# Kernel optimization log

Hardware: AMD Instinct MI355X
Metric: run time of the kernel (lower is better)

## Reference

```python
import jax, jax.numpy as jnp
import numpy as np

C = 0.01            # curvature, hard-coded in the original forward
TEMPERATURE = 0.5
SCALE_BY_TEMPERATURE = True
ARTANH_CLAMP = 1.0 - 1e-5


def setup_inputs() -> dict:
    key = jax.random.key(0)
    k1, k2 = jax.random.split(key)
    B, D = 4096, 128
    features = jax.random.uniform(k1, (B, D), dtype=jnp.float32)
    labels = jax.random.randint(k2, (B,), 0, 32, dtype=jnp.int64)
    return {"features": features, "labels": labels}


def _pairwise_hyp_distance(features):
    # Pair [i, j] in the original: mobius_add(x=-features[j], y=features[i], c)
    # mobius_add(x, y) = (a*x + b*y) / den with
    #   a = 1 + 2c<x,y> + c||y||^2,  b = 1 - c||x||^2,
    #   den = 1 + 2c<x,y> + c^2 ||x||^2 ||y||^2
    # ||a*x + b*y||^2 = a^2||x||^2 + 2ab<x,y> + b^2||y||^2, so the full
    # (B,B,D) broadcast collapses to Gram-matrix algebra (identical math).
    G = features @ features.T                 # [B,B], <f_i, f_j>
    sq = jnp.sum(features * features, axis=-1)  # [B], ||f||^2
    xy = -G                                    # <x,y> with x=-f_j, y=f_i
    x2 = sq[None, :]                           # ||f_j||^2
    y2 = sq[:, None]                           # ||f_i||^2
    a = 1.0 + 2.0 * C * xy + C * y2
    b = 1.0 - C * x2
    den = 1.0 + 2.0 * C * xy + (C * C) * x2 * y2
    num_sq = jnp.maximum(a * a * x2 + 2.0 * a * b * xy + b * b * y2, 0.0)
    norm_diff = jnp.sqrt(C * num_sq) / jnp.abs(den)   # ||sqrt(c)*mobius_add||
    norm_diff = jnp.clip(norm_diff, 0.0, ARTANH_CLAMP)
    return jnp.arctanh(norm_diff) * (2.0 / np.sqrt(C))  # [B,B]


def reference(features, labels):
    B = features.shape[0]
    dist = _pairwise_hyp_distance(features)
    anchor_dot_contrast = -dist / TEMPERATURE
    logits_max = jax.lax.stop_gradient(jnp.max(anchor_dot_contrast, axis=1, keepdims=True))
    logits = anchor_dot_contrast - logits_max
    exp_logits = jnp.exp(logits)

    mask = (labels[:, None] == labels[None, :]).astype(jnp.float32)
    logits_mask = 1.0 - jnp.eye(B, dtype=jnp.float32)
    positives_mask = mask * logits_mask
    negatives_mask = 1.0 - mask

    num_pos = jnp.sum(positives_mask, axis=1)          # [B]
    valid = (num_pos > 0).astype(jnp.float32)
    denominator = (jnp.sum(exp_logits * negatives_mask, axis=1, keepdims=True)
                   + jnp.sum(exp_logits * positives_mask, axis=1, keepdims=True))
    log_probs = logits - jnp.log(denominator)

    row_loss = -jnp.sum(log_probs * positives_mask, axis=1) / jnp.maximum(num_pos, 1.0)
    if SCALE_BY_TEMPERATURE:
        row_loss = row_loss * TEMPERATURE
    row_loss = jnp.where(jnp.isnan(row_loss), 0.0, row_loss)
    n_valid = jnp.sum(valid)
    loss = jnp.sum(row_loss * valid) / jnp.maximum(n_valid, 1.0)
    return loss
```

## Files before the change

### kernel.cpp

```cpp
#include <hip/hip_runtime.h>
#include <cstddef>


typedef __bf16 bf16x8 __attribute__((ext_vector_type(8)));
typedef __bf16 bf16x4 __attribute__((ext_vector_type(4)));
typedef float  f32x4  __attribute__((ext_vector_type(4)));

#define C_CONST 0.01f
#define RATIO_MIN 5.000025e-06f
#define LOGIT_SCALE 13.86294361119890619f
#define TEMP 0.5f
#define LN2 0.69314718055994530942f
constexpr int DD = 128;

__global__ __launch_bounds__(256) void prep_kernel(
    const float* __restrict__ F, __bf16* __restrict__ Fh, float* __restrict__ sq,
    float* __restrict__ denom, float* __restrict__ possum, float* __restrict__ npos) {
  const int tid = threadIdx.x;
  const int lane = tid & 31;
  const int row = blockIdx.x * 8 + (tid >> 5);
  const float4 v = *reinterpret_cast<const float4*>(F + (size_t)row * DD + lane * 4);
  float s = v.x * v.x + v.y * v.y + v.z * v.z + v.w * v.w;
  bf16x4 h;
  h[0] = (__bf16)v.x; h[1] = (__bf16)v.y; h[2] = (__bf16)v.z; h[3] = (__bf16)v.w;
  *reinterpret_cast<bf16x4*>(Fh + (size_t)row * DD + lane * 4) = h;
#pragma unroll
  for (int off = 1; off < 32; off <<= 1) s += __shfl_xor(s, off);
  if (lane == 0) { sq[row] = s; denom[row] = 0.f; possum[row] = 0.f; npos[row] = 0.f; }
}

__global__ __launch_bounds__(256, 4) void gram_kernel(
    const __bf16* __restrict__ Fh,
    const float* __restrict__ sq, const int* __restrict__ labels,
    float* __restrict__ denom, float* __restrict__ possum, float* __restrict__ npos,
    int B) {
  __shared__ __bf16 Bs[128 * 128];
  char* BsB = reinterpret_cast<char*>(Bs);

  const int tid = threadIdx.x;
  const int l  = tid & 63;
  const int w  = tid >> 6;
  const int lg = l >> 4, ln = l & 15;
  const int lx = ln & 7;
  const int row0 = blockIdx.x * 128 + w * 32;
  const int col0 = blockIdx.y * 128;

#pragma unroll
  for (int j = 0; j < 8; ++j) {
    const int k = tid + j * 256;
    const int row = k >> 4;
    const int cc = (k & 15) ^ (row & 7);
    bf16x8 v = *reinterpret_cast<const bf16x8*>(Fh + (size_t)(col0 + row) * DD + cc * 8);
    *reinterpret_cast<bf16x8*>(BsB + (size_t)k * 16) = v;
  }

  const __bf16* Ahp = Fh + (size_t)(row0 + ln) * DD + lg * 8;
  bf16x8 ah[2][4];
#pragma unroll
  for (int fi = 0; fi < 2; ++fi)
#pragma unroll
    for (int kt = 0; kt < 4; ++kt)
      ah[fi][kt] = *reinterpret_cast<const bf16x8*>(Ahp + fi * 16 * DD + kt * 32);

  float si[2][4]; int li[2][4];
#pragma unroll
  for (int fi = 0; fi < 2; ++fi)
#pragma unroll
    for (int r = 0; r < 4; ++r) {
      const int row = row0 + fi * 16 + lg * 4 + r;
      si[fi][r] = sq[row];
      li[fi][r] = labels[row];
    }
  float sqj[8]; int labj[8];
#pragma unroll
  for (int fj = 0; fj < 8; ++fj) {
    sqj[fj]  = sq[col0 + fj * 16 + ln];
    labj[fj] = labels[col0 + fj * 16 + ln];
  }

  __syncthreads();

  float dacc[2][4] = {}, pacc[2][4] = {}, nacc[2][4] = {};

#pragma unroll
  for (int fj = 0; fj < 8; ++fj) {
    const int rbase = (fj * 16 + ln) * 256;
    bf16x8 bh[4];
#pragma unroll
    for (int kt = 0; kt < 4; ++kt)
      bh[kt] = *reinterpret_cast<const bf16x8*>(BsB + rbase + ((((kt * 4 + lg) ^ lx)) << 4));

    f32x4 a0 = (f32x4){0.f, 0.f, 0.f, 0.f};
    f32x4 a1 = (f32x4){0.f, 0.f, 0.f, 0.f};
#pragma unroll
    for (int kt = 0; kt < 4; ++kt) {
      a0 = __builtin_amdgcn_mfma_f32_16x16x32_bf16(ah[0][kt], bh[kt], a0, 0, 0, 0);
      a1 = __builtin_amdgcn_mfma_f32_16x16x32_bf16(ah[1][kt], bh[kt], a1, 0, 0, 0);
    }

    const int col = col0 + fj * 16 + ln;
    const float sjv = sqj[fj];
    const int   ljv = labj[fj];
    const float qv = C_CONST * sjv;
    const float b  = 1.f - qv;
    const float b2 = b * b;
#pragma unroll
    for (int fi = 0; fi < 2; ++fi) {
      const f32x4 av = fi ? a1 : a0;
#pragma unroll
      for (int r = 0; r < 4; ++r) {
        const int row = row0 + fi * 16 + lg * 4 + r;
        const float g   = av[r];
        const float pi_ = C_CONST * si[fi][r];
        const float tt  = fmaf(-2.f * C_CONST, g, 1.f);
        const float a   = tt + pi_;
        const float den = fabsf(fmaf(pi_, qv, tt));
        float ns = a * a * sjv;
        ns = fmaf(b2, si[fi][r], ns);
        ns = fmaf(-2.f * a * b, g, ns);
        ns = fmaxf(ns, 0.f);
        const float rr = __builtin_amdgcn_sqrtf(C_CONST * ns);
        float ratio = (den - rr) * __builtin_amdgcn_rcpf(den + rr);
        ratio = fmaxf(ratio, RATIO_MIN);
        const float P = __builtin_amdgcn_logf(ratio);
        const float t2 = ratio * ratio;
        const float t4 = t2 * t2;
        const float t5 = t4 * ratio;
        const float t10 = t5 * t5;
        const float e = t10 * t10;
        const bool diag = (col == row);
        const bool same = (ljv == li[fi][r]) && !diag;
        dacc[fi][r] += diag ? 0.f : e;
        pacc[fi][r] += same ? LOGIT_SCALE * P : 0.f;
        nacc[fi][r] += same ? 1.f : 0.f;
      }
    }
  }

#pragma unroll
  for (int fi = 0; fi < 2; ++fi)
#pragma unroll
    for (int r = 0; r < 4; ++r) {
      float d = dacc[fi][r], p = pacc[fi][r], n = nacc[fi][r];
#pragma unroll
      for (int off = 1; off < 16; off <<= 1) {
        d += __shfl_xor(d, off);
        p += __shfl_xor(p, off);
        n += __shfl_xor(n, off);
      }
      if (ln == 0) {
        const int row = row0 + fi * 16 + lg * 4 + r;
        atomicAdd(&denom[row], d);
        atomicAdd(&possum[row], p);
        atomicAdd(&npos[row], n);
      }
    }
}

__global__ __launch_bounds__(1024) void finalize_kernel(
    const float* __restrict__ denom, const float* __restrict__ possum,
    const float* __restrict__ npos, float* __restrict__ out, int B) {
  float s_loss = 0.f, s_valid = 0.f;
#pragma unroll
  for (int j = 0; j < 4; ++j) {
    const int i = threadIdx.x + j * 1024;
    const float n = npos[i];
    const float d = denom[i];
    const float p = possum[i];
    if (n > 0.f) {
      float ln_d = __builtin_amdgcn_logf(d) * LN2;
      float rl = -(p - n * ln_d) / n * TEMP;
      if (!(rl != rl)) s_loss += rl;
      s_valid += 1.f;
    }
  }
#pragma unroll
  for (int off = 1; off < 64; off <<= 1) {
    s_loss += __shfl_xor(s_loss, off);
    s_valid += __shfl_xor(s_valid, off);
  }
  __shared__ float red[32];
  const int wid = threadIdx.x >> 6;
  if ((threadIdx.x & 63) == 0) { red[wid] = s_loss; red[wid + 16] = s_valid; }
  __syncthreads();
  if (threadIdx.x == 0) {
    float L = 0.f, V = 0.f;
#pragma unroll
    for (int i = 0; i < 16; ++i) { L += red[i]; V += red[i + 16]; }
    out[0] = L / fmaxf(V, 1.f);
  }
}

extern "C" void kernel_launch(void* const* d_in, const int* in_sizes, int n_in,
                              void* d_out, int out_size, void* d_ws, size_t ws_size,
                              hipStream_t stream) {
  const float* F = (const float*)d_in[0];
  const int* labels = (const int*)d_in[1];
  const int B = in_sizes[1];

  float* sq     = (float*)d_ws;
  float* denom  = sq + B;
  float* possum = denom + B;
  float* npos   = possum + B;
  __bf16* Fh = (__bf16*)(npos + B);

  prep_kernel<<<dim3(B / 8), dim3(256), 0, stream>>>(F, Fh, sq, denom, possum, npos);
  gram_kernel<<<dim3(B / 128, B / 128), dim3(256), 0, stream>>>(
      Fh, sq, labels, denom, possum, npos, B);
  finalize_kernel<<<1, dim3(1024), 0, stream>>>(denom, possum, npos, (float*)d_out, B);
}
```

Measured before the change: 41.15 us.

## Exploit symmetric distance matrix by computing only upper-triangular tiles

The Gram kernel now evaluates only pairs with row < col. It uses a triangular block enumeration of 64-row by 128-column tiles. Each pair's exp, log-prob and positive-count contributions are added both to its row and, through shared-memory column accumulators and atomics, to its column. This roughly halves the per-pair transcendental work and the MFMA work. In exchange it adds per-tile shuffles, a second barrier and twice as many global atomics, and it relies on the hyperbolic distance being exactly symmetric.

```diff
diff --git a/kernel.cpp b/kernel.cpp
--- a/kernel.cpp
+++ b/kernel.cpp
@@ -35,6 +35,7 @@
     float* __restrict__ denom, float* __restrict__ possum, float* __restrict__ npos,
     int B) {
   __shared__ __bf16 Bs[128 * 128];
+  __shared__ float colAcc[4][3][128];
   char* BsB = reinterpret_cast<char*>(Bs);
 
   const int tid = threadIdx.x;
@@ -42,8 +43,15 @@
   const int w  = tid >> 6;
   const int lg = l >> 4, ln = l & 15;
   const int lx = ln & 7;
-  const int row0 = blockIdx.x * 128 + w * 32;
-  const int col0 = blockIdx.y * 128;
+
+  const int t = blockIdx.x;
+  int bj = (int)((sqrtf((float)(4 * t + 1)) - 1.f) * 0.5f);
+  while (bj * bj + bj > t) --bj;
+  while ((bj + 1) * (bj + 1) + (bj + 1) <= t) ++bj;
+  const int bi = t - (bj * bj + bj);
+
+  const int row0 = bi * 64 + w * 16;
+  const int col0 = bj * 128;
 
 #pragma unroll
   for (int j = 0; j < 8; ++j) {
@@ -55,22 +63,18 @@
   }
 
   const __bf16* Ahp = Fh + (size_t)(row0 + ln) * DD + lg * 8;
-  bf16x8 ah[2][4];
-#pragma unroll
-  for (int fi = 0; fi < 2; ++fi)
-#pragma unroll
-    for (int kt = 0; kt < 4; ++kt)
-      ah[fi][kt] = *reinterpret_cast<const bf16x8*>(Ahp + fi * 16 * DD + kt * 32);
-
-  float si[2][4]; int li[2][4];
-#pragma unroll
-  for (int fi = 0; fi < 2; ++fi)
-#pragma unroll
-    for (int r = 0; r < 4; ++r) {
-      const int row = row0 + fi * 16 + lg * 4 + r;
-      si[fi][r] = sq[row];
-      li[fi][r] = labels[row];
-    }
+  bf16x8 ah[4];
+#pragma unroll
+  for (int kt = 0; kt < 4; ++kt)
+    ah[kt] = *reinterpret_cast<const bf16x8*>(Ahp + kt * 32);
+
+  float si[4]; int li[4];
+#pragma unroll
+  for (int r = 0; r < 4; ++r) {
+    const int row = row0 + lg * 4 + r;
+    si[r] = sq[row];
+    li[r] = labels[row];
+  }
   float sqj[8]; int labj[8];
 #pragma unroll
   for (int fj = 0; fj < 8; ++fj) {
@@ -80,7 +84,7 @@
 
   __syncthreads();
 
-  float dacc[2][4] = {}, pacc[2][4] = {}, nacc[2][4] = {};
+  float dacc[4] = {}, pacc[4] = {}, nacc[4] = {};
 
 #pragma unroll
   for (int fj = 0; fj < 8; ++fj) {
@@ -90,13 +94,10 @@
     for (int kt = 0; kt < 4; ++kt)
       bh[kt] = *reinterpret_cast<const bf16x8*>(BsB + rbase + ((((kt * 4 + lg) ^ lx)) << 4));
 
-    f32x4 a0 = (f32x4){0.f, 0.f, 0.f, 0.f};
-    f32x4 a1 = (f32x4){0.f, 0.f, 0.f, 0.f};
-#pragma unroll
-    for (int kt = 0; kt < 4; ++kt) {
-      a0 = __builtin_amdgcn_mfma_f32_16x16x32_bf16(ah[0][kt], bh[kt], a0, 0, 0, 0);
-      a1 = __builtin_amdgcn_mfma_f32_16x16x32_bf16(ah[1][kt], bh[kt], a1, 0, 0, 0);
-    }
+    f32x4 acc = (f32x4){0.f, 0.f, 0.f, 0.f};
+#pragma unroll
+    for (int kt = 0; kt < 4; ++kt)
+      acc = __builtin_amdgcn_mfma_f32_16x16x32_bf16(ah[kt], bh[kt], acc, 0, 0, 0);
 
     const int col = col0 + fj * 16 + ln;
     const float sjv = sqj[fj];
@@ -104,57 +105,72 @@
     const float qv = C_CONST * sjv;
     const float b  = 1.f - qv;
     const float b2 = b * b;
-#pragma unroll
-    for (int fi = 0; fi < 2; ++fi) {
-      const f32x4 av = fi ? a1 : a0;
-#pragma unroll
-      for (int r = 0; r < 4; ++r) {
-        const int row = row0 + fi * 16 + lg * 4 + r;
-        const float g   = av[r];
-        const float pi_ = C_CONST * si[fi][r];
-        const float tt  = fmaf(-2.f * C_CONST, g, 1.f);
-        const float a   = tt + pi_;
-        const float den = fabsf(fmaf(pi_, qv, tt));
-        float ns = a * a * sjv;
-        ns = fmaf(b2, si[fi][r], ns);
-        ns = fmaf(-2.f * a * b, g, ns);
-        ns = fmaxf(ns, 0.f);
-        const float rr = __builtin_amdgcn_sqrtf(C_CONST * ns);
-        float ratio = (den - rr) * __builtin_amdgcn_rcpf(den + rr);
-        ratio = fmaxf(ratio, RATIO_MIN);
-        const float P = __builtin_amdgcn_logf(ratio);
-        const float t2 = ratio * ratio;
-        const float t4 = t2 * t2;
-        const float t5 = t4 * ratio;
-        const float t10 = t5 * t5;
-        const float e = t10 * t10;
-        const bool diag = (col == row);
-        const bool same = (ljv == li[fi][r]) && !diag;
-        dacc[fi][r] += diag ? 0.f : e;
-        pacc[fi][r] += same ? LOGIT_SCALE * P : 0.f;
-        nacc[fi][r] += same ? 1.f : 0.f;
-      }
-    }
-  }
-
-#pragma unroll
-  for (int fi = 0; fi < 2; ++fi)
+    float cd = 0.f, cp = 0.f, cn = 0.f;
 #pragma unroll
     for (int r = 0; r < 4; ++r) {
-      float d = dacc[fi][r], p = pacc[fi][r], n = nacc[fi][r];
-#pragma unroll
-      for (int off = 1; off < 16; off <<= 1) {
-        d += __shfl_xor(d, off);
-        p += __shfl_xor(p, off);
-        n += __shfl_xor(n, off);
-      }
-      if (ln == 0) {
-        const int row = row0 + fi * 16 + lg * 4 + r;
-        atomicAdd(&denom[row], d);
-        atomicAdd(&possum[row], p);
-        atomicAdd(&npos[row], n);
-      }
-    }
+      const int row = row0 + lg * 4 + r;
+      const float g   = acc[r];
+      const float pi_ = C_CONST * si[r];
+      const float tt  = fmaf(-2.f * C_CONST, g, 1.f);
+      const float a   = tt + pi_;
+      const float den = fabsf(fmaf(pi_, qv, tt));
+      float ns = a * a * sjv;
+      ns = fmaf(b2, si[r], ns);
+      ns = fmaf(-2.f * a * b, g, ns);
+      ns = fmaxf(ns, 0.f);
+      const float rr = __builtin_amdgcn_sqrtf(C_CONST * ns);
+      float ratio = (den - rr) * __builtin_amdgcn_rcpf(den + rr);
+      ratio = fmaxf(ratio, RATIO_MIN);
+      const float P = __builtin_amdgcn_logf(ratio);
+      const float t2 = ratio * ratio;
+      const float t4 = t2 * t2;
+      const float t5 = t4 * ratio;
+      const float t10 = t5 * t5;
+      const float e = t10 * t10;
+      const bool mask = row < col;
+      const bool same = mask && (ljv == li[r]);
+      const float ev = mask ? e : 0.f;
+      const float pv = same ? LOGIT_SCALE * P : 0.f;
+      const float nv = same ? 1.f : 0.f;
+      dacc[r] += ev; pacc[r] += pv; nacc[r] += nv;
+      cd += ev; cp += pv; cn += nv;
+    }
+    cd += __shfl_xor(cd, 16); cd += __shfl_xor(cd, 32);
+    cp += __shfl_xor(cp, 16); cp += __shfl_xor(cp, 32);
+    cn += __shfl_xor(cn, 16); cn += __shfl_xor(cn, 32);
+    if (l < 16) {
+      colAcc[w][0][fj * 16 + ln] = cd;
+      colAcc[w][1][fj * 16 + ln] = cp;
+      colAcc[w][2][fj * 16 + ln] = cn;
+    }
+  }
+
+#pragma unroll
+  for (int r = 0; r < 4; ++r) {
+    float d = dacc[r], p = pacc[r], n = nacc[r];
+#pragma unroll
+    for (int off = 1; off < 16; off <<= 1) {
+      d += __shfl_xor(d, off);
+      p += __shfl_xor(p, off);
+      n += __shfl_xor(n, off);
+    }
+    if (ln == 0) {
+      const int row = row0 + lg * 4 + r;
+      atomicAdd(&denom[row], d);
+      atomicAdd(&possum[row], p);
+      atomicAdd(&npos[row], n);
+    }
+  }
+
+  __syncthreads();
+  if (tid < 128) {
+    const float d = colAcc[0][0][tid] + colAcc[1][0][tid] + colAcc[2][0][tid] + colAcc[3][0][tid];
+    const float p = colAcc[0][1][tid] + colAcc[1][1][tid] + colAcc[2][1][tid] + colAcc[3][1][tid];
+    const float n = colAcc[0][2][tid] + colAcc[1][2][tid] + colAcc[2][2][tid] + colAcc[3][2][tid];
+    atomicAdd(&denom[col0 + tid], d);
+    atomicAdd(&possum[col0 + tid], p);
+    atomicAdd(&npos[col0 + tid], n);
+  }
 }
 
 __global__ __launch_bounds__(1024) void finalize_kernel(
@@ -204,8 +220,11 @@
   float* npos   = possum + B;
   __bf16* Fh = (__bf16*)(npos + B);
 
+  const int nbj = B / 128;
+  const int nblocks = nbj * nbj + nbj;
+
   prep_kernel<<<dim3(B / 8), dim3(256), 0, stream>>>(F, Fh, sq, denom, possum, npos);
-  gram_kernel<<<dim3(B / 128, B / 128), dim3(256), 0, stream>>>(
+  gram_kernel<<<dim3(nblocks), dim3(256), 0, stream>>>(
       Fh, sq, labels, denom, possum, npos, B);
   finalize_kernel<<<1, dim3(1024), 0, stream>>>(denom, possum, npos, (float*)d_out, B);
 }
```

New measurement: 40.49 us. No clear change (-1.6%).
